# Kernel optimization log

Hardware: AMD Instinct MI355X
Metric: run time of the kernel (lower is better)

## Reference

```python
import jax, jax.numpy as jnp
import numpy as np

B, T, C = 2, 2048, 1024
NH = 16
HD = C // NH


def setup_inputs() -> dict:
    key = jax.random.key(0)
    k1, k2, k3 = jax.random.split(key, 3)
    x = jax.random.normal(k1, (B, T, C), dtype=jnp.float32)
    w_qkv = jax.random.normal(k2, (C, 3 * C), dtype=jnp.float32) * (C ** -0.5)
    w_proj = jax.random.normal(k3, (C, C), dtype=jnp.float32) * (C ** -0.5)
    return {"x": x, "w_qkv": w_qkv, "w_proj": w_proj}


def reference(x, w_qkv, w_proj):
    Bv, Tv, Cv = x.shape
    qkv = x @ w_qkv  # [B, T, 3C]
    q, k, v = jnp.split(qkv, 3, axis=-1)
    # [B, T, C] -> [B, NH, T, HD]
    q = q.reshape(Bv, Tv, NH, HD).transpose(0, 2, 1, 3)
    k = k.reshape(Bv, Tv, NH, HD).transpose(0, 2, 1, 3)
    v = v.reshape(Bv, Tv, NH, HD).transpose(0, 2, 1, 3)
    att = jnp.einsum("bhqd,bhkd->bhqk", q, k) * (HD ** -0.5)
    causal = jnp.tril(jnp.ones((Tv, Tv), dtype=bool))  # [T, T]
    att = jnp.where(causal[None, None, :, :], att, -jnp.inf)
    att = jax.nn.softmax(att, axis=-1)
    # dropout p=0.0 (eval) -> identity
    y = jnp.einsum("bhqk,bhkd->bhqd", att, v)  # [B, NH, T, HD]
    y = y.transpose(0, 2, 1, 3).reshape(Bv, Tv, Cv)
    return y @ w_proj
```

## Files before the change

kernel.cpp:

```cpp
#include <hip/hip_runtime.h>
#include <hip/hip_bf16.h>

#define B_ 2
#define T_ 2048
#define C_ 1024
#define NH_ 16
#define HD_ 64

using bf16 = __hip_bfloat16;
typedef __attribute__((ext_vector_type(8))) short bf16x8;
typedef __attribute__((ext_vector_type(4))) float f32x4;

__device__ __forceinline__ float bf2f(unsigned short u) {
    union { unsigned int i; float f; } v;
    v.i = ((unsigned int)u) << 16;
    return v.f;
}
__device__ __forceinline__ unsigned short f2bf(float f) {
    union { float f; unsigned int u; } v;
    v.f = f;
    unsigned int r = v.u + 0x7fffu + ((v.u >> 16) & 1u);
    return (unsigned short)(r >> 16);
}
__device__ __forceinline__ unsigned int cvt_pk_bf16(float lo, float hi) {
    unsigned int r;
    asm("v_cvt_pk_bf16_f32 %0, %1, %2" : "=v"(r) : "v"(lo), "v"(hi));
    return r;
}
__device__ __forceinline__ void gld_lds16(const void* g, void* l) {
    __builtin_amdgcn_global_load_lds(
        (__attribute__((address_space(1))) void*)g,
        (__attribute__((address_space(3))) void*)l, 16, 0, 0);
}

__global__ __launch_bounds__(256) void prep(
    const float* __restrict__ X, const float* __restrict__ Wq,
    unsigned short* __restrict__ Xb, unsigned short* __restrict__ Wqt) {
    __shared__ short S[64][72];
    const int b = blockIdx.x;
    const int t = threadIdx.x;
    if (b < 2048) {
        int i = (b * 256 + t) * 8;
        float4 f0 = *reinterpret_cast<const float4*>(&X[i]);
        float4 f1 = *reinterpret_cast<const float4*>(&X[i + 4]);
        union { unsigned short s[8]; uint4 v; } o;
        o.s[0] = f2bf(f0.x); o.s[1] = f2bf(f0.y); o.s[2] = f2bf(f0.z); o.s[3] = f2bf(f0.w);
        o.s[4] = f2bf(f1.x); o.s[5] = f2bf(f1.y); o.s[6] = f2bf(f1.z); o.s[7] = f2bf(f1.w);
        *reinterpret_cast<uint4*>(&Xb[i]) = o.v;
        return;
    }
    const int idx = b - 2048;
    const int n0 = (idx % 48) * 64, k0 = (idx / 48) * 64;
    const int NN = 3 * C_, KK = C_;
    const int lr = t >> 2, lc = (t & 3) * 16;
    const float* src = &Wq[(size_t)(k0 + lr) * NN + n0 + lc];
    #pragma unroll
    for (int j4 = 0; j4 < 4; ++j4) {
        float4 f = *reinterpret_cast<const float4*>(src + j4 * 4);
        S[lc + j4 * 4 + 0][lr] = (short)f2bf(f.x);
        S[lc + j4 * 4 + 1][lr] = (short)f2bf(f.y);
        S[lc + j4 * 4 + 2][lr] = (short)f2bf(f.z);
        S[lc + j4 * 4 + 3][lr] = (short)f2bf(f.w);
    }
    __syncthreads();
    union { unsigned short s[16]; uint4 v[2]; } o;
    #pragma unroll
    for (int j = 0; j < 16; ++j) o.s[j] = (unsigned short)S[lr][lc + j];
    unsigned short* dst = &Wqt[(size_t)(n0 + lr) * KK + k0 + lc];
    *reinterpret_cast<uint4*>(dst)     = o.v[0];
    *reinterpret_cast<uint4*>(dst + 8) = o.v[1];
}

__global__ __launch_bounds__(256) void post(
    const unsigned short* __restrict__ V, unsigned short* __restrict__ Vt,
    const float* __restrict__ Wp, unsigned short* __restrict__ Wpt) {
    __shared__ short S[64][72];
    const int b = blockIdx.x;
    const int t = threadIdx.x;
    const int lr = t >> 2, lc = (t & 3) * 16;
    if (b < 1024) {
        const int bh = b >> 5, t0 = (b & 31) * 64;
        const unsigned short* src = V + ((size_t)bh * T_ + t0 + lr) * HD_ + lc;
        union { uint4 v[2]; unsigned short s[16]; } u;
        u.v[0] = *reinterpret_cast<const uint4*>(src);
        u.v[1] = *reinterpret_cast<const uint4*>(src + 8);
        #pragma unroll
        for (int j = 0; j < 16; ++j) S[lc + j][lr] = (short)u.s[j];
        __syncthreads();
        union { unsigned short s[16]; uint4 v[2]; } o;
        #pragma unroll
        for (int j = 0; j < 16; ++j) o.s[j] = (unsigned short)S[lr][lc + j];
        unsigned short* dst = Vt + ((size_t)bh * HD_ + lr) * T_ + t0 + lc;
        *reinterpret_cast<uint4*>(dst)     = o.v[0];
        *reinterpret_cast<uint4*>(dst + 8) = o.v[1];
        return;
    }
    const int idx = b - 1024;
    const int n0 = (idx & 15) * 64, k0 = (idx >> 4) * 64;
    const float* src = &Wp[(size_t)(k0 + lr) * C_ + n0 + lc];
    #pragma unroll
    for (int j4 = 0; j4 < 4; ++j4) {
        float4 f = *reinterpret_cast<const float4*>(src + j4 * 4);
        S[lc + j4 * 4 + 0][lr] = (short)f2bf(f.x);
        S[lc + j4 * 4 + 1][lr] = (short)f2bf(f.y);
        S[lc + j4 * 4 + 2][lr] = (short)f2bf(f.z);
        S[lc + j4 * 4 + 3][lr] = (short)f2bf(f.w);
    }
    __syncthreads();
    union { unsigned short s[16]; uint4 v[2]; } o;
    #pragma unroll
    for (int j = 0; j < 16; ++j) o.s[j] = (unsigned short)S[lr][lc + j];
    unsigned short* dst = &Wpt[(size_t)(n0 + lr) * C_ + k0 + lc];
    *reinterpret_cast<uint4*>(dst)     = o.v[0];
    *reinterpret_cast<uint4*>(dst + 8) = o.v[1];
}

__global__ __launch_bounds__(256) void qkv_gemm_mfma(
    const unsigned short* __restrict__ A, const unsigned short* __restrict__ Bt,
    unsigned short* __restrict__ Qb, unsigned short* __restrict__ Kb,
    unsigned short* __restrict__ Vb) {
    __shared__ short As[128 * 32];
    __shared__ short Bs[128 * 32];
    const int t = threadIdx.x;
    const int wid = t >> 6, lane = t & 63;
    const int wm = wid >> 1, wn = wid & 1;
    const int c = lane & 15, g = lane >> 4;
    const int dd = blockIdx.x;
    const int w  = (dd & 7) * 96 + (dd >> 3);
    const int m0 = (w / 24) * 128, n0 = (w % 24) * 128;
    const int K = C_;
    const int srow = t >> 2, skk = (t & 3) * 8;

    f32x4 acc[4][4];
    #pragma unroll
    for (int i = 0; i < 4; ++i)
        #pragma unroll
        for (int j = 0; j < 4; ++j) acc[i][j] = (f32x4){0.f, 0.f, 0.f, 0.f};

    for (int k0 = 0; k0 < K; k0 += 32) {
        __syncthreads();
        gld_lds16(&A[(size_t)(m0 + srow) * K + k0 + skk],       As + t * 8);
        gld_lds16(&A[(size_t)(m0 + 64 + srow) * K + k0 + skk],  As + 2048 + t * 8);
        gld_lds16(&Bt[(size_t)(n0 + srow) * K + k0 + skk],      Bs + t * 8);
        gld_lds16(&Bt[(size_t)(n0 + 64 + srow) * K + k0 + skk], Bs + 2048 + t * 8);
        __syncthreads();
        bf16x8 af[4], bfv[4];
        #pragma unroll
        for (int mi = 0; mi < 4; ++mi)
            af[mi] = *reinterpret_cast<const bf16x8*>(&As[(wm * 64 + mi * 16 + c) * 32 + g * 8]);
        #pragma unroll
        for (int ni = 0; ni < 4; ++ni)
            bfv[ni] = *reinterpret_cast<const bf16x8*>(&Bs[(wn * 64 + ni * 16 + c) * 32 + g * 8]);
        #pragma unroll
        for (int mi = 0; mi < 4; ++mi)
            #pragma unroll
            for (int ni = 0; ni < 4; ++ni)
                acc[mi][ni] = __builtin_amdgcn_mfma_f32_16x16x32_bf16(af[mi], bfv[ni], acc[mi][ni], 0, 0, 0);
    }

    const int nbase = n0 + wn * 64;
    const int which = nbase >> 10;
    const int h     = (nbase >> 6) & (NH_ - 1);
    const float scale = (which == 0) ? 0.125f * 1.44269504f : 1.0f;
    unsigned short* dst = (which == 0) ? Qb : ((which == 1) ? Kb : Vb);
    #pragma unroll
    for (int mi = 0; mi < 4; ++mi)
        #pragma unroll
        for (int r = 0; r < 4; ++r) {
            const int m = m0 + wm * 64 + mi * 16 + 4 * g + r;
            const int bb = m >> 11, tq = m & (T_ - 1);
            unsigned short* p = dst + ((size_t)((bb << 4) | h) * T_ + tq) * HD_;
            #pragma unroll
            for (int ni = 0; ni < 4; ++ni)
                p[ni * 16 + c] = f2bf(acc[mi][ni][r] * scale);
        }
}

__global__ __launch_bounds__(256) void proj_gemm_mfma(
    const unsigned short* __restrict__ A, const unsigned short* __restrict__ Bt,
    float* __restrict__ Out) {
    __shared__ short As[64 * 32];
    __shared__ short Bs[128 * 32];
    const int t = threadIdx.x;
    const int wid = t >> 6, lane = t & 63;
    const int wm = wid >> 1, wn = wid & 1;
    const int c = lane & 15, g = lane >> 4;
    const int m0 = blockIdx.y * 64, n0 = blockIdx.x * 128;
    const int K = C_;
    const int srow = t >> 2, skk = (t & 3) * 8;

    f32x4 acc[2][4];
    #pragma unroll
    for (int i = 0; i < 2; ++i)
        #pragma unroll
        for (int j = 0; j < 4; ++j) acc[i][j] = (f32x4){0.f, 0.f, 0.f, 0.f};

    for (int k0 = 0; k0 < K; k0 += 32) {
        __syncthreads();
        gld_lds16(&A[(size_t)(m0 + srow) * K + k0 + skk],       As + t * 8);
        gld_lds16(&Bt[(size_t)(n0 + srow) * K + k0 + skk],      Bs + t * 8);
        gld_lds16(&Bt[(size_t)(n0 + 64 + srow) * K + k0 + skk], Bs + 2048 + t * 8);
        __syncthreads();
        bf16x8 af[2], bfv[4];
        #pragma unroll
        for (int mi = 0; mi < 2; ++mi)
            af[mi] = *reinterpret_cast<const bf16x8*>(&As[(wm * 32 + mi * 16 + c) * 32 + g * 8]);
        #pragma unroll
        for (int ni = 0; ni < 4; ++ni)
            bfv[ni] = *reinterpret_cast<const bf16x8*>(&Bs[(wn * 64 + ni * 16 + c) * 32 + g * 8]);
        #pragma unroll
        for (int mi = 0; mi < 2; ++mi)
            #pragma unroll
            for (int ni = 0; ni < 4; ++ni)
                acc[mi][ni] = __builtin_amdgcn_mfma_f32_16x16x32_bf16(af[mi], bfv[ni], acc[mi][ni], 0, 0, 0);
    }

    #pragma unroll
    for (int mi = 0; mi < 2; ++mi)
        #pragma unroll
        for (int r = 0; r < 4; ++r) {
            const int m = m0 + wm * 32 + mi * 16 + 4 * g + r;
            float* p = Out + (size_t)m * C_ + n0 + wn * 64;
            #pragma unroll
            for (int ni = 0; ni < 4; ++ni)
                p[ni * 16 + c] = acc[mi][ni][r];
        }
}

__global__ __launch_bounds__(512) void attn_mfma(
    const unsigned short* __restrict__ Qb, const unsigned short* __restrict__ Kb,
    const unsigned short* __restrict__ Vt_g, unsigned short* __restrict__ Yu) {
    __shared__ short Ks[2][64][72];
    __shared__ short Vt[2][64][72];

    const int t    = threadIdx.x;
    const int wid  = t >> 6;
    const int lane = t & 63;
    const int c    = lane & 15;
    const int g    = lane >> 4;

    const int d   = blockIdx.x;
    const int xcd = d & 7;
    const int tt  = d >> 3;
    const int up  = tt & 15;
    const int k2  = tt >> 4;
    const int bh  = (k2 << 3) | xcd;
    const int u   = (k2 & 2) ? (15 - up) : up;
    const int qtB = 2 * u + 1;
    const int myqt = (wid < 4) ? (2 * u) : qtB;

    const int bb = bh >> 4, h = bh & (NH_ - 1);
    const int qw0 = (wid & 3) * 16;
    const int q0  = myqt * 64;

    const unsigned short* Qh  = Qb   + (size_t)bh * T_ * HD_;
    const unsigned short* Kh  = Kb   + (size_t)bh * T_ * HD_;
    const unsigned short* VTh = Vt_g + (size_t)bh * HD_ * T_;

    const int srow = t >> 3, scol = (t & 7) * 8;
    const int jA = scol, jB = scol + 4;
    const int slotA = 32 * (jA >> 5) + 8 * ((jA >> 2) & 3) + 4 * ((jA >> 4) & 1);
    const int slotB = 32 * (jB >> 5) + 8 * ((jB >> 2) & 3) + 4 * ((jB >> 4) & 1);

    bf16x8 qf0, qf1;
    {
        const unsigned short* qs = Qh + (size_t)(q0 + qw0 + c) * HD_ + g * 8;
        qf0 = *reinterpret_cast<const bf16x8*>(qs);
        qf1 = *reinterpret_cast<const bf16x8*>(qs + 32);
    }

    float l_run = 0.f;
    f32x4 yacc[4];
    #pragma unroll
    for (int nt = 0; nt < 4; ++nt) yacc[nt] = (f32x4){0.f, 0.f, 0.f, 0.f};

    uint4 kv, vv;
    {
        kv = *reinterpret_cast<const uint4*>(&Kh[(size_t)srow * HD_ + scol]);
        vv = *reinterpret_cast<const uint4*>(&VTh[(size_t)srow * T_ + scol]);
    }

    #pragma unroll 1
    for (int kt = 0; kt <= qtB; ++kt) {
        const int cur = kt & 1;
        *reinterpret_cast<uint4*>(&Ks[cur][srow][scol]) = kv;
        *reinterpret_cast<uint2*>(&Vt[cur][srow][slotA]) = make_uint2(vv.x, vv.y);
        *reinterpret_cast<uint2*>(&Vt[cur][srow][slotB]) = make_uint2(vv.z, vv.w);
        __syncthreads();

        if (kt < qtB) {
            const int j1 = (kt + 1) * 64;
            kv = *reinterpret_cast<const uint4*>(&Kh[(size_t)(j1 + srow) * HD_ + scol]);
            vv = *reinterpret_cast<const uint4*>(&VTh[(size_t)srow * T_ + j1 + scol]);
        }

        if (kt <= myqt) {
            f32x4 sacc[4];
            #pragma unroll
            for (int nt = 0; nt < 4; ++nt) sacc[nt] = (f32x4){0.f, 0.f, 0.f, 0.f};
            __builtin_amdgcn_s_setprio(1);
            #pragma unroll
            for (int kk = 0; kk < 2; ++kk) {
                const bf16x8 qf = kk ? qf1 : qf0;
                #pragma unroll
                for (int nt = 0; nt < 4; ++nt) {
                    bf16x8 kf = *reinterpret_cast<const bf16x8*>(&Ks[cur][nt * 16 + c][kk * 32 + g * 8]);
                    sacc[nt] = __builtin_amdgcn_mfma_f32_16x16x32_bf16(kf, qf, sacc[nt], 0, 0, 0);
                }
            }
            __builtin_amdgcn_s_setprio(0);

            const bool diag = (kt == myqt);
            float p[4][4];
            float lsum = 0.f;
            #pragma unroll
            for (int nt = 0; nt < 4; ++nt)
                #pragma unroll
                for (int r = 0; r < 4; ++r) {
                    float s = sacc[nt][r];
                    if (diag && (nt * 16 + 4 * g + r > qw0 + c)) s = -1e30f;
                    float pv = exp2f(s);
                    p[nt][r] = pv;
                    lsum += pv;
                }
            l_run += lsum;

            unsigned int pk[8];
            #pragma unroll
            for (int nt = 0; nt < 4; ++nt) {
                pk[2 * nt]     = cvt_pk_bf16(p[nt][0], p[nt][1]);
                pk[2 * nt + 1] = cvt_pk_bf16(p[nt][2], p[nt][3]);
            }

            __builtin_amdgcn_s_setprio(1);
            #pragma unroll
            for (int kk = 0; kk < 2; ++kk) {
                union { unsigned int w[4]; bf16x8 v; } pa;
                pa.w[0] = pk[4 * kk + 0]; pa.w[1] = pk[4 * kk + 1];
                pa.w[2] = pk[4 * kk + 2]; pa.w[3] = pk[4 * kk + 3];
                #pragma unroll
                for (int nt = 0; nt < 4; ++nt) {
                    bf16x8 vb = *reinterpret_cast<const bf16x8*>(&Vt[cur][nt * 16 + c][kk * 32 + g * 8]);
                    yacc[nt] = __builtin_amdgcn_mfma_f32_16x16x32_bf16(pa.v, vb, yacc[nt], 0, 0, 0);
                }
            }
            __builtin_amdgcn_s_setprio(0);
        }
    }

    float lf = l_run;
    lf += __shfl_xor(lf, 16, 64);
    lf += __shfl_xor(lf, 32, 64);
    const float inv = 1.0f / lf;
    const int ii = __float_as_int(inv);
    float invr[4];
    #pragma unroll
    for (int r = 0; r < 4; ++r)
        invr[r] = __int_as_float(__builtin_amdgcn_ds_bpermute((4 * g + r) * 4, ii));
    #pragma unroll
    for (int r = 0; r < 4; ++r) {
        const size_t row = (size_t)(bb * T_ + q0 + qw0 + 4 * g + r);
        #pragma unroll
        for (int nt = 0; nt < 4; ++nt) {
            const int col = h * HD_ + 16 * nt + c;
            Yu[row * C_ + col] = f2bf(yacc[nt][r] * invr[r]);
        }
    }
}

extern "C" void kernel_launch(void* const* d_in, const int* in_sizes, int n_in,
                              void* d_out, int out_size, void* d_ws, size_t ws_size,
                              hipStream_t stream) {
    const float* x      = (const float*)d_in[0];
    const float* w_qkv  = (const float*)d_in[1];
    const float* w_proj = (const float*)d_in[2];
    float* out = (float*)d_out;

    const size_t HELEMS = (size_t)B_ * NH_ * T_ * HD_;
    unsigned short* Qb   = (unsigned short*)d_ws;
    unsigned short* Kb   = Qb + HELEMS;
    unsigned short* Vraw = Kb + HELEMS;
    unsigned short* Yb   = Vraw;
    unsigned short* Xb   = Vraw + HELEMS;
    unsigned short* Vt   = Xb;
    unsigned short* Wqt  = Xb + HELEMS;
    unsigned short* Wpt  = Wqt;

    prep<<<2816, 256, 0, stream>>>(x, w_qkv, Xb, Wqt);
    qkv_gemm_mfma<<<768, 256, 0, stream>>>(Xb, Wqt, Qb, Kb, Vraw);
    post<<<1280, 256, 0, stream>>>(Vraw, Vt, w_proj, Wpt);
    attn_mfma<<<512, 512, 0, stream>>>(Qb, Kb, Vt, Yb);
    proj_gemm_mfma<<<dim3(8, 64), 256, 0, stream>>>(Yb, Wpt, out);
}
```

Measured before the change: 112.8 us.

## Split long causal attention rows across two blocks with atomic-flag merge

The attention kernel changes from 512 blocks of 8 waves, each pairing two query tiles, to 1536 blocks of 4 waves, each handling one query tile. Query tiles in the second half of the sequence have their key range split between two blocks. Each half writes unnormalized partial outputs and row sums to workspace, and the second block to finish (found through an atomic counter reset in prep) combines them and normalizes. This evens out the causal load imbalance and raises parallelism. The cost is extra global traffic for partials, a bf16 rounding of the partial accumulator, single-buffered K/V shared memory with an extra barrier per iteration, and reliance on workspace beyond the earlier layout.

```diff
diff --git a/kernel.cpp b/kernel.cpp
--- a/kernel.cpp
+++ b/kernel.cpp
@@ -35,10 +35,15 @@
 
 __global__ __launch_bounds__(256) void prep(
     const float* __restrict__ X, const float* __restrict__ Wq,
-    unsigned short* __restrict__ Xb, unsigned short* __restrict__ Wqt) {
+    unsigned short* __restrict__ Xb, unsigned short* __restrict__ Wqt,
+    int* __restrict__ flags) {
     __shared__ short S[64][72];
     const int b = blockIdx.x;
     const int t = threadIdx.x;
+    if (b == 2816) {
+        for (int i = t; i < 512; i += 256) flags[i] = 0;
+        return;
+    }
     if (b < 2048) {
         int i = (b * 256 + t) * 8;
         float4 f0 = *reinterpret_cast<const float4*>(&X[i]);
@@ -227,11 +232,14 @@
         }
 }
 
-__global__ __launch_bounds__(512) void attn_mfma(
+__global__ __launch_bounds__(256) void attn_mfma(
     const unsigned short* __restrict__ Qb, const unsigned short* __restrict__ Kb,
-    const unsigned short* __restrict__ Vt_g, unsigned short* __restrict__ Yu) {
-    __shared__ short Ks[2][64][72];
-    __shared__ short Vt[2][64][72];
+    const unsigned short* __restrict__ Vt_g, unsigned short* __restrict__ Yu,
+    unsigned short* __restrict__ Ypart, float* __restrict__ Lpart,
+    int* __restrict__ flags) {
+    __shared__ short Ks[64][72];
+    __shared__ short Vt[64][72];
+    __shared__ int who;
 
     const int t    = threadIdx.x;
     const int wid  = t >> 6;
@@ -239,28 +247,48 @@
     const int c    = lane & 15;
     const int g    = lane >> 4;
 
-    const int d   = blockIdx.x;
-    const int xcd = d & 7;
-    const int tt  = d >> 3;
-    const int up  = tt & 15;
-    const int k2  = tt >> 4;
-    const int bh  = (k2 << 3) | xcd;
-    const int u   = (k2 & 2) ? (15 - up) : up;
-    const int qtB = 2 * u + 1;
-    const int myqt = (wid < 4) ? (2 * u) : qtB;
+    const int d = blockIdx.x;
+    int bh, qt, kLo, kHi, pidx;
+    if (d < 512) {
+        const int xcd = d & 7;
+        const int u0  = (d >> 3) & 15;
+        const int k2  = d >> 7;
+        const int u   = (k2 & 2) ? (15 - u0) : u0;
+        bh = (k2 << 3) | xcd;
+        qt = u; kLo = 0; kHi = qt + 1; pidx = -1;
+    } else {
+        const int e    = d - 512;
+        const int xcd  = e & 7;
+        const int gi   = e >> 3;
+        const int k2   = gi & 3;
+        const int w    = gi >> 2;
+        const int v8   = w & 7;
+        const int j    = w >> 3;
+        const int v    = (j >= 2) ? (15 - v8) : v8;
+        const int hx   = j & 1;
+        bh = (k2 << 3) | xcd;
+        qt = 16 + v;
+        const int L = (18 + v) >> 1;
+        kLo = hx ? L : 0;
+        kHi = hx ? (qt + 1) : L;
+        pidx = ((bh * 16 + v) << 1) | hx;
+    }
 
     const int bb = bh >> 4, h = bh & (NH_ - 1);
-    const int qw0 = (wid & 3) * 16;
-    const int q0  = myqt * 64;
+    const int q0 = qt * 64;
+    const int qw0 = wid * 16;
 
     const unsigned short* Qh  = Qb   + (size_t)bh * T_ * HD_;
     const unsigned short* Kh  = Kb   + (size_t)bh * T_ * HD_;
     const unsigned short* VTh = Vt_g + (size_t)bh * HD_ * T_;
 
-    const int srow = t >> 3, scol = (t & 7) * 8;
-    const int jA = scol, jB = scol + 4;
-    const int slotA = 32 * (jA >> 5) + 8 * ((jA >> 2) & 3) + 4 * ((jA >> 4) & 1);
-    const int slotB = 32 * (jB >> 5) + 8 * ((jB >> 2) & 3) + 4 * ((jB >> 4) & 1);
+    const int srow = t >> 2, scol = (t & 3) * 16;
+    int slot[4];
+    #pragma unroll
+    for (int x = 0; x < 4; ++x) {
+        const int j = scol + 4 * x;
+        slot[x] = 32 * (j >> 5) + 8 * ((j >> 2) & 3) + 4 * ((j >> 4) & 1);
+    }
 
     bf16x8 qf0, qf1;
     {
@@ -274,96 +302,159 @@
     #pragma unroll
     for (int nt = 0; nt < 4; ++nt) yacc[nt] = (f32x4){0.f, 0.f, 0.f, 0.f};
 
-    uint4 kv, vv;
+    uint4 kv0, kv1, vv0, vv1;
     {
-        kv = *reinterpret_cast<const uint4*>(&Kh[(size_t)srow * HD_ + scol]);
-        vv = *reinterpret_cast<const uint4*>(&VTh[(size_t)srow * T_ + scol]);
+        const unsigned short* ks = &Kh[(size_t)(kLo * 64 + srow) * HD_ + scol];
+        kv0 = *reinterpret_cast<const uint4*>(ks);
+        kv1 = *reinterpret_cast<const uint4*>(ks + 8);
+        const unsigned short* vs = &VTh[(size_t)srow * T_ + kLo * 64 + scol];
+        vv0 = *reinterpret_cast<const uint4*>(vs);
+        vv1 = *reinterpret_cast<const uint4*>(vs + 8);
     }
 
     #pragma unroll 1
-    for (int kt = 0; kt <= qtB; ++kt) {
-        const int cur = kt & 1;
-        *reinterpret_cast<uint4*>(&Ks[cur][srow][scol]) = kv;
-        *reinterpret_cast<uint2*>(&Vt[cur][srow][slotA]) = make_uint2(vv.x, vv.y);
-        *reinterpret_cast<uint2*>(&Vt[cur][srow][slotB]) = make_uint2(vv.z, vv.w);
-        __syncthreads();
-
-        if (kt < qtB) {
+    for (int kt = kLo; kt < kHi; ++kt) {
+        __syncthreads();
+        *reinterpret_cast<uint4*>(&Ks[srow][scol])      = kv0;
+        *reinterpret_cast<uint4*>(&Ks[srow][scol + 8])  = kv1;
+        *reinterpret_cast<uint2*>(&Vt[srow][slot[0]]) = make_uint2(vv0.x, vv0.y);
+        *reinterpret_cast<uint2*>(&Vt[srow][slot[1]]) = make_uint2(vv0.z, vv0.w);
+        *reinterpret_cast<uint2*>(&Vt[srow][slot[2]]) = make_uint2(vv1.x, vv1.y);
+        *reinterpret_cast<uint2*>(&Vt[srow][slot[3]]) = make_uint2(vv1.z, vv1.w);
+        __syncthreads();
+
+        if (kt + 1 < kHi) {
             const int j1 = (kt + 1) * 64;
-            kv = *reinterpret_cast<const uint4*>(&Kh[(size_t)(j1 + srow) * HD_ + scol]);
-            vv = *reinterpret_cast<const uint4*>(&VTh[(size_t)srow * T_ + j1 + scol]);
-        }
-
-        if (kt <= myqt) {
-            f32x4 sacc[4];
-            #pragma unroll
-            for (int nt = 0; nt < 4; ++nt) sacc[nt] = (f32x4){0.f, 0.f, 0.f, 0.f};
-            __builtin_amdgcn_s_setprio(1);
-            #pragma unroll
-            for (int kk = 0; kk < 2; ++kk) {
-                const bf16x8 qf = kk ? qf1 : qf0;
-                #pragma unroll
-                for (int nt = 0; nt < 4; ++nt) {
-                    bf16x8 kf = *reinterpret_cast<const bf16x8*>(&Ks[cur][nt * 16 + c][kk * 32 + g * 8]);
-                    sacc[nt] = __builtin_amdgcn_mfma_f32_16x16x32_bf16(kf, qf, sacc[nt], 0, 0, 0);
-                }
+            const unsigned short* ks = &Kh[(size_t)(j1 + srow) * HD_ + scol];
+            kv0 = *reinterpret_cast<const uint4*>(ks);
+            kv1 = *reinterpret_cast<const uint4*>(ks + 8);
+            const unsigned short* vs = &VTh[(size_t)srow * T_ + j1 + scol];
+            vv0 = *reinterpret_cast<const uint4*>(vs);
+            vv1 = *reinterpret_cast<const uint4*>(vs + 8);
+        }
+
+        f32x4 sacc[4];
+        #pragma unroll
+        for (int nt = 0; nt < 4; ++nt) sacc[nt] = (f32x4){0.f, 0.f, 0.f, 0.f};
+        __builtin_amdgcn_s_setprio(1);
+        #pragma unroll
+        for (int kk = 0; kk < 2; ++kk) {
+            const bf16x8 qf = kk ? qf1 : qf0;
+            #pragma unroll
+            for (int nt = 0; nt < 4; ++nt) {
+                bf16x8 kf = *reinterpret_cast<const bf16x8*>(&Ks[nt * 16 + c][kk * 32 + g * 8]);
+                sacc[nt] = __builtin_amdgcn_mfma_f32_16x16x32_bf16(kf, qf, sacc[nt], 0, 0, 0);
             }
-            __builtin_amdgcn_s_setprio(0);
-
-            const bool diag = (kt == myqt);
-            float p[4][4];
-            float lsum = 0.f;
+        }
+        __builtin_amdgcn_s_setprio(0);
+
+        float p[4][4];
+        float lsum = 0.f;
+        if (kt == qt) {
             #pragma unroll
             for (int nt = 0; nt < 4; ++nt)
                 #pragma unroll
                 for (int r = 0; r < 4; ++r) {
                     float s = sacc[nt][r];
-                    if (diag && (nt * 16 + 4 * g + r > qw0 + c)) s = -1e30f;
+                    if (nt * 16 + 4 * g + r > qw0 + c) s = -1e30f;
                     float pv = exp2f(s);
                     p[nt][r] = pv;
                     lsum += pv;
                 }
-            l_run += lsum;
-
-            unsigned int pk[8];
+        } else {
+            #pragma unroll
+            for (int nt = 0; nt < 4; ++nt)
+                #pragma unroll
+                for (int r = 0; r < 4; ++r) {
+                    float pv = exp2f(sacc[nt][r]);
+                    p[nt][r] = pv;
+                    lsum += pv;
+                }
+        }
+        l_run += lsum;
+
+        unsigned int pk[8];
+        #pragma unroll
+        for (int nt = 0; nt < 4; ++nt) {
+            pk[2 * nt]     = cvt_pk_bf16(p[nt][0], p[nt][1]);
+            pk[2 * nt + 1] = cvt_pk_bf16(p[nt][2], p[nt][3]);
+        }
+
+        __builtin_amdgcn_s_setprio(1);
+        #pragma unroll
+        for (int kk = 0; kk < 2; ++kk) {
+            union { unsigned int w[4]; bf16x8 v; } pa;
+            pa.w[0] = pk[4 * kk + 0]; pa.w[1] = pk[4 * kk + 1];
+            pa.w[2] = pk[4 * kk + 2]; pa.w[3] = pk[4 * kk + 3];
             #pragma unroll
             for (int nt = 0; nt < 4; ++nt) {
-                pk[2 * nt]     = cvt_pk_bf16(p[nt][0], p[nt][1]);
-                pk[2 * nt + 1] = cvt_pk_bf16(p[nt][2], p[nt][3]);
+                bf16x8 vb = *reinterpret_cast<const bf16x8*>(&Vt[nt * 16 + c][kk * 32 + g * 8]);
+                yacc[nt] = __builtin_amdgcn_mfma_f32_16x16x32_bf16(pa.v, vb, yacc[nt], 0, 0, 0);
             }
-
-            __builtin_amdgcn_s_setprio(1);
-            #pragma unroll
-            for (int kk = 0; kk < 2; ++kk) {
-                union { unsigned int w[4]; bf16x8 v; } pa;
-                pa.w[0] = pk[4 * kk + 0]; pa.w[1] = pk[4 * kk + 1];
-                pa.w[2] = pk[4 * kk + 2]; pa.w[3] = pk[4 * kk + 3];
-                #pragma unroll
-                for (int nt = 0; nt < 4; ++nt) {
-                    bf16x8 vb = *reinterpret_cast<const bf16x8*>(&Vt[cur][nt * 16 + c][kk * 32 + g * 8]);
-                    yacc[nt] = __builtin_amdgcn_mfma_f32_16x16x32_bf16(pa.v, vb, yacc[nt], 0, 0, 0);
-                }
-            }
-            __builtin_amdgcn_s_setprio(0);
-        }
+        }
+        __builtin_amdgcn_s_setprio(0);
     }
 
     float lf = l_run;
     lf += __shfl_xor(lf, 16, 64);
     lf += __shfl_xor(lf, 32, 64);
-    const float inv = 1.0f / lf;
-    const int ii = __float_as_int(inv);
-    float invr[4];
-    #pragma unroll
-    for (int r = 0; r < 4; ++r)
-        invr[r] = __int_as_float(__builtin_amdgcn_ds_bpermute((4 * g + r) * 4, ii));
+
+    if (pidx < 0) {
+        const float inv = 1.0f / lf;
+        const int ii = __float_as_int(inv);
+        float invr[4];
+        #pragma unroll
+        for (int r = 0; r < 4; ++r)
+            invr[r] = __int_as_float(__builtin_amdgcn_ds_bpermute((4 * g + r) * 4, ii));
+        #pragma unroll
+        for (int r = 0; r < 4; ++r) {
+            const size_t row = (size_t)(bb * T_ + q0 + qw0 + 4 * g + r);
+            #pragma unroll
+            for (int nt = 0; nt < 4; ++nt) {
+                const int col = h * HD_ + 16 * nt + c;
+                Yu[row * C_ + col] = f2bf(yacc[nt][r] * invr[r]);
+            }
+        }
+        return;
+    }
+
+    if (lane < 16 && wid == (t >> 6))
+        ;
+    if (lane < 16)
+        Lpart[pidx * 64 + qw0 + lane] = lf;
     #pragma unroll
     for (int r = 0; r < 4; ++r) {
-        const size_t row = (size_t)(bb * T_ + q0 + qw0 + 4 * g + r);
-        #pragma unroll
-        for (int nt = 0; nt < 4; ++nt) {
-            const int col = h * HD_ + 16 * nt + c;
-            Yu[row * C_ + col] = f2bf(yacc[nt][r] * invr[r]);
+        const int qrow = qw0 + 4 * g + r;
+        #pragma unroll
+        for (int nt = 0; nt < 4; ++nt)
+            Ypart[(size_t)pidx * 4096 + qrow * 64 + 16 * nt + c] = f2bf(yacc[nt][r]);
+    }
+    __threadfence();
+    __syncthreads();
+    if (t == 0)
+        who = __hip_atomic_fetch_add(&flags[pidx >> 1], 1,
+                                     __ATOMIC_ACQ_REL, __HIP_MEMORY_SCOPE_AGENT);
+    __syncthreads();
+    if (who == 1) {
+        const int pp = pidx ^ 1;
+        const float lf2 = lf + Lpart[pp * 64 + qw0 + c];
+        const float inv = 1.0f / lf2;
+        const int ii = __float_as_int(inv);
+        float invr[4];
+        #pragma unroll
+        for (int r = 0; r < 4; ++r)
+            invr[r] = __int_as_float(__builtin_amdgcn_ds_bpermute((4 * g + r) * 4, ii));
+        #pragma unroll
+        for (int r = 0; r < 4; ++r) {
+            const int qrow = qw0 + 4 * g + r;
+            const size_t row = (size_t)(bb * T_ + q0 + qrow);
+            #pragma unroll
+            for (int nt = 0; nt < 4; ++nt) {
+                const int col = h * HD_ + 16 * nt + c;
+                const float ym = yacc[nt][r] +
+                    bf2f(Ypart[(size_t)pp * 4096 + qrow * 64 + 16 * nt + c]);
+                Yu[row * C_ + col] = f2bf(ym * invr[r]);
+            }
         }
     }
 }
@@ -377,18 +468,21 @@
     float* out = (float*)d_out;
 
     const size_t HELEMS = (size_t)B_ * NH_ * T_ * HD_;
-    unsigned short* Qb   = (unsigned short*)d_ws;
-    unsigned short* Kb   = Qb + HELEMS;
-    unsigned short* Vraw = Kb + HELEMS;
-    unsigned short* Yb   = Vraw;
-    unsigned short* Xb   = Vraw + HELEMS;
-    unsigned short* Vt   = Xb;
-    unsigned short* Wqt  = Xb + HELEMS;
-    unsigned short* Wpt  = Wqt;
-
-    prep<<<2816, 256, 0, stream>>>(x, w_qkv, Xb, Wqt);
+    unsigned short* Qb    = (unsigned short*)d_ws;
+    unsigned short* Kb    = Qb + HELEMS;
+    unsigned short* Vraw  = Kb + HELEMS;
+    unsigned short* Yb    = Vraw;
+    unsigned short* Xb    = Vraw + HELEMS;
+    unsigned short* Vt    = Xb;
+    unsigned short* Wqt   = Xb + HELEMS;
+    unsigned short* Wpt   = Wqt;
+    unsigned short* Ypart = Wqt + (size_t)3 * C_ * C_;
+    float*          Lpart = (float*)(Ypart + (size_t)1024 * 4096);
+    int*            flags = (int*)(Lpart + 1024 * 64);
+
+    prep<<<2817, 256, 0, stream>>>(x, w_qkv, Xb, Wqt, flags);
     qkv_gemm_mfma<<<768, 256, 0, stream>>>(Xb, Wqt, Qb, Kb, Vraw);
     post<<<1280, 256, 0, stream>>>(Vraw, Vt, w_proj, Wpt);
-    attn_mfma<<<512, 512, 0, stream>>>(Qb, Kb, Vt, Yb);
+    attn_mfma<<<1536, 256, 0, stream>>>(Qb, Kb, Vt, Yb, Ypart, Lpart, flags);
     proj_gemm_mfma<<<dim3(8, 64), 256, 0, stream>>>(Yb, Wpt, out);
 }
```

Result: slower. 268.4 us (+137.9%).

## Double-buffer LDS tiles in QKV and projection GEMMs to overlap loads

Applied to the files above, without the earlier changes.

Both bf16 MFMA GEMM kernels now keep two LDS buffers for the A and B tiles. The first K-tile is prefetched before the loop, and each iteration issues the global-to-LDS load for the next tile before computing on the current one. This overlaps memory latency with MFMA work and needs only one barrier per K-step instead of two. In exchange, LDS use per block doubles, which may lower occupancy, and correctness relies on the barrier waiting for the outstanding direct-to-LDS loads.

```diff
diff --git a/kernel.cpp b/kernel.cpp
--- a/kernel.cpp
+++ b/kernel.cpp
@@ -119,8 +119,8 @@
     const unsigned short* __restrict__ A, const unsigned short* __restrict__ Bt,
     unsigned short* __restrict__ Qb, unsigned short* __restrict__ Kb,
     unsigned short* __restrict__ Vb) {
-    __shared__ short As[128 * 32];
-    __shared__ short Bs[128 * 32];
+    __shared__ short As[2][128 * 32];
+    __shared__ short Bs[2][128 * 32];
     const int t = threadIdx.x;
     const int wid = t >> 6, lane = t & 63;
     const int wm = wid >> 1, wn = wid & 1;
@@ -137,20 +137,29 @@
         #pragma unroll
         for (int j = 0; j < 4; ++j) acc[i][j] = (f32x4){0.f, 0.f, 0.f, 0.f};
 
-    for (int k0 = 0; k0 < K; k0 += 32) {
+    gld_lds16(&A[(size_t)(m0 + srow) * K + skk],       As[0] + t * 8);
+    gld_lds16(&A[(size_t)(m0 + 64 + srow) * K + skk],  As[0] + 2048 + t * 8);
+    gld_lds16(&Bt[(size_t)(n0 + srow) * K + skk],      Bs[0] + t * 8);
+    gld_lds16(&Bt[(size_t)(n0 + 64 + srow) * K + skk], Bs[0] + 2048 + t * 8);
+
+    #pragma unroll 1
+    for (int kt = 0; kt < 32; ++kt) {
+        const int cur = kt & 1;
         __syncthreads();
-        gld_lds16(&A[(size_t)(m0 + srow) * K + k0 + skk],       As + t * 8);
-        gld_lds16(&A[(size_t)(m0 + 64 + srow) * K + k0 + skk],  As + 2048 + t * 8);
-        gld_lds16(&Bt[(size_t)(n0 + srow) * K + k0 + skk],      Bs + t * 8);
-        gld_lds16(&Bt[(size_t)(n0 + 64 + srow) * K + k0 + skk], Bs + 2048 + t * 8);
-        __syncthreads();
+        if (kt < 31) {
+            const int k0 = (kt + 1) * 32;
+            gld_lds16(&A[(size_t)(m0 + srow) * K + k0 + skk],       As[cur ^ 1] + t * 8);
+            gld_lds16(&A[(size_t)(m0 + 64 + srow) * K + k0 + skk],  As[cur ^ 1] + 2048 + t * 8);
+            gld_lds16(&Bt[(size_t)(n0 + srow) * K + k0 + skk],      Bs[cur ^ 1] + t * 8);
+            gld_lds16(&Bt[(size_t)(n0 + 64 + srow) * K + k0 + skk], Bs[cur ^ 1] + 2048 + t * 8);
+        }
         bf16x8 af[4], bfv[4];
         #pragma unroll
         for (int mi = 0; mi < 4; ++mi)
-            af[mi] = *reinterpret_cast<const bf16x8*>(&As[(wm * 64 + mi * 16 + c) * 32 + g * 8]);
+            af[mi] = *reinterpret_cast<const bf16x8*>(&As[cur][(wm * 64 + mi * 16 + c) * 32 + g * 8]);
         #pragma unroll
         for (int ni = 0; ni < 4; ++ni)
-            bfv[ni] = *reinterpret_cast<const bf16x8*>(&Bs[(wn * 64 + ni * 16 + c) * 32 + g * 8]);
+            bfv[ni] = *reinterpret_cast<const bf16x8*>(&Bs[cur][(wn * 64 + ni * 16 + c) * 32 + g * 8]);
         #pragma unroll
         for (int mi = 0; mi < 4; ++mi)
             #pragma unroll
@@ -179,8 +188,8 @@
 __global__ __launch_bounds__(256) void proj_gemm_mfma(
     const unsigned short* __restrict__ A, const unsigned short* __restrict__ Bt,
     float* __restrict__ Out) {
-    __shared__ short As[64 * 32];
-    __shared__ short Bs[128 * 32];
+    __shared__ short As[2][64 * 32];
+    __shared__ short Bs[2][128 * 32];
     const int t = threadIdx.x;
     const int wid = t >> 6, lane = t & 63;
     const int wm = wid >> 1, wn = wid & 1;
@@ -195,19 +204,27 @@
         #pragma unroll
         for (int j = 0; j < 4; ++j) acc[i][j] = (f32x4){0.f, 0.f, 0.f, 0.f};
 
-    for (int k0 = 0; k0 < K; k0 += 32) {
+    gld_lds16(&A[(size_t)(m0 + srow) * K + skk],       As[0] + t * 8);
+    gld_lds16(&Bt[(size_t)(n0 + srow) * K + skk],      Bs[0] + t * 8);
+    gld_lds16(&Bt[(size_t)(n0 + 64 + srow) * K + skk], Bs[0] + 2048 + t * 8);
+
+    #pragma unroll 1
+    for (int kt = 0; kt < 32; ++kt) {
+        const int cur = kt & 1;
         __syncthreads();
-        gld_lds16(&A[(size_t)(m0 + srow) * K + k0 + skk],       As + t * 8);
-        gld_lds16(&Bt[(size_t)(n0 + srow) * K + k0 + skk],      Bs + t * 8);
-        gld_lds16(&Bt[(size_t)(n0 + 64 + srow) * K + k0 + skk], Bs + 2048 + t * 8);
-        __syncthreads();
+        if (kt < 31) {
+            const int k0 = (kt + 1) * 32;
+            gld_lds16(&A[(size_t)(m0 + srow) * K + k0 + skk],       As[cur ^ 1] + t * 8);
+            gld_lds16(&Bt[(size_t)(n0 + srow) * K + k0 + skk],      Bs[cur ^ 1] + t * 8);
+            gld_lds16(&Bt[(size_t)(n0 + 64 + srow) * K + k0 + skk], Bs[cur ^ 1] + 2048 + t * 8);
+        }
         bf16x8 af[2], bfv[4];
         #pragma unroll
         for (int mi = 0; mi < 2; ++mi)
-            af[mi] = *reinterpret_cast<const bf16x8*>(&As[(wm * 32 + mi * 16 + c) * 32 + g * 8]);
+            af[mi] = *reinterpret_cast<const bf16x8*>(&As[cur][(wm * 32 + mi * 16 + c) * 32 + g * 8]);
         #pragma unroll
         for (int ni = 0; ni < 4; ++ni)
-            bfv[ni] = *reinterpret_cast<const bf16x8*>(&Bs[(wn * 64 + ni * 16 + c) * 32 + g * 8]);
+            bfv[ni] = *reinterpret_cast<const bf16x8*>(&Bs[cur][(wn * 64 + ni * 16 + c) * 32 + g * 8]);
         #pragma unroll
         for (int mi = 0; mi < 2; ++mi)
             #pragma unroll
```

Measured after the change: 113.6 us. Within noise of the previous version (+0.7%).
